# Optimization experiments

Hardware: AMD Instinct MI355X
Metric: run time of the kernel (lower is better)

Reference implementation:

```python
import jax, jax.numpy as jnp
import numpy as np

E, K = 8, 2            # num_experts, top_k
D, H = 1024, 4096      # d_model, expert_hidden_dim
B, S = 4, 2048         # batch, seq
AUX_W = 0.01


def setup_inputs() -> dict:
    key = jax.random.key(0)
    k0, k1, k2, k3 = jax.random.split(key, 4)
    return {
        "x": jax.random.normal(k0, (B, S, D), jnp.float32),
        "router_w": jax.random.normal(k1, (D, E), jnp.float32) * 0.02,  # normal(0.02) init per MoERouter
        "router_b": jnp.zeros((E,), jnp.float32),
        "w_up": jax.random.normal(k2, (E, D, H), jnp.float32) * (1.0 / np.sqrt(D)),
        "b_up": jnp.zeros((E, H), jnp.float32),
        "w_down": jax.random.normal(k3, (E, H, D), jnp.float32) * (1.0 / np.sqrt(H)),
        "b_down": jnp.zeros((E, D), jnp.float32),
    }


def reference(x, router_w, router_b, w_up, b_up, w_down, b_down):
    # Router
    logits = x @ router_w + router_b                       # (B,S,E)
    router_probs = jax.nn.softmax(logits, axis=-1)         # (B,S,E)
    topk_logits, topk_idx = jax.lax.top_k(logits, K)       # (B,S,K)
    topk_p = jax.nn.softmax(topk_logits, axis=-1)          # (B,S,K)

    # Dense all-expert MLP (matches original: every expert computed on every token)
    h = jax.nn.gelu(jnp.einsum('bsd,edh->bseh', x, w_up) + b_up)   # (B,S,E,H)
    all_out = jnp.einsum('bseh,ehd->bsed', h, w_down) + b_down     # (B,S,E,D)

    # Top-k gather + weighted combine
    sel = jnp.take_along_axis(all_out, topk_idx[..., None], axis=2)  # (B,S,K,D)
    output = jnp.sum(topk_p[..., None] * sel, axis=2)                # (B,S,D)

    # Load-balancing aux loss (Switch/Mixtral formulation)
    counts = jnp.zeros((E,), jnp.float32).at[topk_idx.reshape(-1)].add(1.0)
    fraction = counts / (B * S * K)
    prob_mean = router_probs.mean(axis=(0, 1))
    aux_loss = E * jnp.sum(fraction * prob_mean) * AUX_W
    return output, aux_loss, router_probs
```

## Files before the change

kernel.cpp:

```cpp
#include <hip/hip_runtime.h>
#include <hip/hip_bf16.h>
#include <stdint.h>

constexpr int NT = 8192;
constexpr int NE = 8;
constexpr int ND = 1024;
constexpr int NH = 4096;

constexpr int TM = 128;
constexpr int TN = 256;
constexpr int BK = 32;

typedef __attribute__((ext_vector_type(8))) short short8;
typedef __attribute__((ext_vector_type(4))) float f32x4;

constexpr size_t O_XBF  = 0;
constexpr size_t O_WUPT = O_XBF  + (size_t)NT * ND * 2;
constexpr size_t O_WDNT = O_WUPT + (size_t)NE * NH * ND * 2;
constexpr size_t O_HBUF = O_WDNT + (size_t)NE * ND * NH * 2;
constexpr size_t O_STOK = O_HBUF + (size_t)NT * 2 * NH * 2;
constexpr size_t O_SP   = O_STOK + (size_t)NT * 2 * 4;
constexpr size_t O_TKE  = O_SP   + (size_t)NT * 2 * 4;
constexpr size_t O_TKP  = O_TKE  + (size_t)NT * 2 * 4;
constexpr size_t O_CTRL = O_TKP  + (size_t)NT * 2 * 4;
constexpr size_t O_TLUP = O_CTRL + 272;
constexpr size_t O_TLDN = O_TLUP + 160 * 4;

__device__ __forceinline__ void gl_lds16(const void* g, void* l) {
  using GP = char __attribute__((address_space(1))) *;
  using LP = char __attribute__((address_space(3))) *;
  __builtin_amdgcn_global_load_lds((GP)(uintptr_t)g, (LP)(uint32_t)(uintptr_t)l, 16, 0, 0);
}

__device__ __forceinline__ float fast_gelu(float x) {
  float u  = 0.7978845608028654f * (x + 0.044715f * x * x * x);
  float ex = __expf(2.0f * u);
  float th = 1.0f - 2.0f / (ex + 1.0f);
  return 0.5f * x * (1.0f + th);
}

__global__ __launch_bounds__(256) void moe_router(
    const float* __restrict__ x, const float* __restrict__ rw, const float* __restrict__ rb,
    __hip_bfloat16* __restrict__ xbf,
    float* __restrict__ probs_out, int* __restrict__ topk_e, float* __restrict__ topk_p,
    int* __restrict__ cnt_ek, float* __restrict__ probsum)
{
  __shared__ float ps[NE];
  __shared__ int cs[16];
  const int tid = threadIdx.x;
  if (tid < NE) ps[tid] = 0.f;
  if (tid < 16) cs[tid] = 0;
  __syncthreads();
  const int lane = tid & 63, wv = tid >> 6;
  for (int it = 0; it < 8; ++it) {
    const int t = blockIdx.x * 4 + wv + it * 1024;
    const float* xr = x + (size_t)t * ND;
    float acc[NE] = {};
#pragma unroll 4
    for (int j = 0; j < 16; ++j) {
      const int d = j * 64 + lane;
      const float xv = xr[d];
      xbf[(size_t)t * ND + d] = __float2bfloat16(xv);
      const float* w = rw + (size_t)d * NE;
#pragma unroll
      for (int ee = 0; ee < NE; ++ee) acc[ee] += xv * w[ee];
    }
#pragma unroll
    for (int ee = 0; ee < NE; ++ee)
#pragma unroll
      for (int off = 32; off >= 1; off >>= 1)
        acc[ee] += __shfl_down(acc[ee], off, 64);
    if (lane == 0) {
      float lg[NE];
#pragma unroll
      for (int ee = 0; ee < NE; ++ee) lg[ee] = acc[ee] + rb[ee];
      float mx = lg[0];
#pragma unroll
      for (int ee = 1; ee < NE; ++ee) mx = fmaxf(mx, lg[ee]);
      float s = 0.f, pe[NE];
#pragma unroll
      for (int ee = 0; ee < NE; ++ee) { pe[ee] = __expf(lg[ee] - mx); s += pe[ee]; }
      const float inv = 1.f / s;
#pragma unroll
      for (int ee = 0; ee < NE; ++ee) {
        const float pr = pe[ee] * inv;
        probs_out[(size_t)t * NE + ee] = pr;
        atomicAdd(&ps[ee], pr);
      }
      int i1 = 0; float l1 = lg[0];
#pragma unroll
      for (int ee = 1; ee < NE; ++ee) if (lg[ee] > l1) { l1 = lg[ee]; i1 = ee; }
      int i2 = 0; float l2 = -3.0e38f;
#pragma unroll
      for (int ee = 0; ee < NE; ++ee) if (ee != i1 && lg[ee] > l2) { l2 = lg[ee]; i2 = ee; }
      const float e2 = __expf(l2 - l1);
      const float dn = 1.f + e2;
      topk_e[t * 2]     = i1;  topk_e[t * 2 + 1] = i2;
      topk_p[t * 2]     = 1.f / dn;
      topk_p[t * 2 + 1] = e2 / dn;
      atomicAdd(&cs[i1 * 2], 1);
      atomicAdd(&cs[i2 * 2 + 1], 1);
    }
  }
  __syncthreads();
  if (tid < NE) atomicAdd(&probsum[tid], ps[tid]);
  if (tid < 16) atomicAdd(&cnt_ek[tid], cs[tid]);
}

__global__ void moe_finalize(const int* __restrict__ cnt_ek, int* __restrict__ off_ek,
                             const float* __restrict__ probsum, float* __restrict__ aux_out,
                             int* __restrict__ ntiles, int* __restrict__ tl_up,
                             int* __restrict__ tl_dn)
{
  __shared__ int c[16], off[16], uoff[8], ucnt[8], doff[16], dcnt[16];
  const int tid = threadIdx.x;
  if (tid < 16) c[tid] = cnt_ek[tid];
  __syncthreads();
  if (tid == 0) {
    int run = 0;
    for (int i = 0; i < 16; ++i) { off[i] = run; run += c[i]; }
    int ur = 0;
    for (int e = 0; e < NE; ++e) {
      ucnt[e] = (c[2 * e] + c[2 * e + 1] + TM - 1) / TM;
      uoff[e] = ur; ur += ucnt[e];
    }
    ntiles[0] = ur;
    int dr = 0;
    for (int i = 0; i < 16; ++i) {
      dcnt[i] = (c[i] + TM - 1) / TM;
      doff[i] = dr; dr += dcnt[i];
    }
    ntiles[1] = dr;
    float aux = 0.f;
    for (int e = 0; e < NE; ++e) {
      float frac = (float)(c[2 * e] + c[2 * e + 1]) / (float)(NT * 2);
      aux += frac * (probsum[e] / (float)NT);
    }
    aux_out[0] = (float)NE * aux * 0.01f;
  }
  __syncthreads();
  if (tid < 16) off_ek[tid] = off[tid];
  if (tid < 8)
    for (int mb = 0; mb < ucnt[tid]; ++mb) tl_up[uoff[tid] + mb] = (tid << 16) | mb;
  if (tid >= 32 && tid < 48) {
    const int i = tid - 32;
    for (int mb = 0; mb < dcnt[i]; ++mb) tl_dn[doff[i] + mb] = (i << 16) | mb;
  }
}

__global__ __launch_bounds__(256) void moe_scatter(
    const int* __restrict__ topk_e, const float* __restrict__ topk_p,
    const int* __restrict__ off_ek, int* __restrict__ fill_ek,
    int* __restrict__ slot_token, float* __restrict__ slot_p)
{
  __shared__ int lc[16], gb[16], offs[16];
  const int tid = threadIdx.x;
  if (tid < 16) lc[tid] = 0;
  __syncthreads();
  const int t = blockIdx.x * 256 + tid;
  const int id0 = topk_e[t * 2] * 2;
  const int id1 = topk_e[t * 2 + 1] * 2 + 1;
  atomicAdd(&lc[id0], 1);
  atomicAdd(&lc[id1], 1);
  __syncthreads();
  if (tid < 16) {
    gb[tid] = atomicAdd(&fill_ek[tid], lc[tid]);
    offs[tid] = off_ek[tid];
    lc[tid] = 0;
  }
  __syncthreads();
  {
    const int r = atomicAdd(&lc[id0], 1);
    const int slot = offs[id0] + gb[id0] + r;
    slot_token[slot] = t;
    slot_p[slot] = topk_p[t * 2];
  }
  {
    const int r = atomicAdd(&lc[id1], 1);
    const int slot = offs[id1] + gb[id1] + r;
    slot_token[slot] = t;
    slot_p[slot] = topk_p[t * 2 + 1];
  }
}

__global__ __launch_bounds__(256) void moe_transpose_cast(
    const float* __restrict__ in, __hip_bfloat16* __restrict__ outp, int Adim, int Bdim)
{
  __shared__ unsigned short tile[64 * 66];
  const int e = blockIdx.z;
  const int b0 = blockIdx.x * 64, a0 = blockIdx.y * 64;
  const float* ip = in + (size_t)e * Adim * Bdim + (size_t)a0 * Bdim + b0;
  const int c4 = (threadIdx.x & 15) * 4;
  const int r0 = threadIdx.x >> 4;
#pragma unroll
  for (int i = 0; i < 4; ++i) {
    const int r = r0 + i * 16;
    const float4 v = *(const float4*)(ip + (size_t)r * Bdim + c4);
    ushort4 u;
    u.x = __hip_bfloat16_raw(__float2bfloat16(v.x)).x;
    u.y = __hip_bfloat16_raw(__float2bfloat16(v.y)).x;
    u.z = __hip_bfloat16_raw(__float2bfloat16(v.z)).x;
    u.w = __hip_bfloat16_raw(__float2bfloat16(v.w)).x;
    *(ushort4*)&tile[r * 66 + c4] = u;
  }
  __syncthreads();
  unsigned short* op = (unsigned short*)outp + (size_t)e * Bdim * Adim + (size_t)b0 * Adim + a0;
  const int cc  = threadIdx.x >> 2;
  const int rr0 = (threadIdx.x & 3) * 16;
  unsigned short u[16];
#pragma unroll
  for (int i = 0; i < 16; ++i) u[i] = tile[(rr0 + i) * 66 + cc];
  *(short8*)(op + (size_t)cc * Adim + rr0)     = *(short8*)&u[0];
  *(short8*)(op + (size_t)cc * Adim + rr0 + 8) = *(short8*)&u[8];
}

__global__ __launch_bounds__(512, 4) void moe_gemm_up(
    const __hip_bfloat16* __restrict__ xbf,
    const __hip_bfloat16* __restrict__ wupT,
    const float* __restrict__ b_up,
    const int* __restrict__ slot_token,
    const int* __restrict__ cnt_ek, const int* __restrict__ off_ek,
    const int* __restrict__ ntiles, const int* __restrict__ tl_up,
    __hip_bfloat16* __restrict__ hbuf)
{
  if ((int)blockIdx.y >= ntiles[0]) return;
  const int tl = tl_up[blockIdx.y];
  const int e = tl >> 16, mb = tl & 0xffff;
  const int cnt = cnt_ek[2 * e] + cnt_ek[2 * e + 1];
  const int base = off_ek[2 * e];
  const int m0 = mb * TM;
  const int n0 = blockIdx.x * TN;
  const int valid = (cnt - m0 < TM) ? (cnt - m0) : TM;

  __shared__ __align__(16) __hip_bfloat16 As[TM * BK];
  __shared__ __align__(16) __hip_bfloat16 Bs[TN * BK];

  const int tid = threadIdx.x;
  const int lane = tid & 63, wv = tid >> 6;

  const int raA = tid >> 2;
  const int kcA = ((tid & 3) ^ ((raA >> 1) & 3)) * 8;
  int srA = m0 + raA; if (srA >= cnt) srA = cnt - 1;
  const __hip_bfloat16* ga = xbf + (size_t)slot_token[base + srA] * ND + kcA;
  const __hip_bfloat16* gb[2];
#pragma unroll
  for (int j = 0; j < 2; ++j) {
    const int ci = tid + 512 * j;
    const int row = ci >> 2;
    const int kc = ((ci & 3) ^ ((row >> 1) & 3)) * 8;
    gb[j] = wupT + ((size_t)e * NH + n0 + row) * ND + kc;
  }
  char* lA = (char*)As + tid * 16;
  char* lB = (char*)Bs + tid * 16;

  const int wm = (wv >> 2) * 64, wn = (wv & 3) * 64;
  const int l15 = lane & 15, q = lane >> 4;
  const int ssw = (q ^ ((l15 >> 1) & 3)) * 16;
  const char* rA = (const char*)As + (wm + l15) * 64 + ssw;
  const char* rB = (const char*)Bs + (wn + l15) * 64 + ssw;

  f32x4 acc[4][4] = {};

  for (int kk = 0; kk < ND; kk += BK) {
    __syncthreads();
    gl_lds16(ga + kk, lA);
    gl_lds16(gb[0] + kk, lB);
    gl_lds16(gb[1] + kk, lB + 8192);
    __syncthreads();
    short8 af[4], bfr[4];
#pragma unroll
    for (int i = 0; i < 4; ++i) af[i]  = *(const short8*)(rA + i * 1024);
#pragma unroll
    for (int i = 0; i < 4; ++i) bfr[i] = *(const short8*)(rB + i * 1024);
#pragma unroll
    for (int mt = 0; mt < 4; ++mt)
#pragma unroll
      for (int nt = 0; nt < 4; ++nt)
        acc[mt][nt] = __builtin_amdgcn_mfma_f32_16x16x32_bf16(af[mt], bfr[nt], acc[mt][nt], 0, 0, 0);
  }

  float bias[4];
#pragma unroll
  for (int nt = 0; nt < 4; ++nt) bias[nt] = b_up[e * NH + n0 + wn + nt * 16 + l15];
#pragma unroll
  for (int mt = 0; mt < 4; ++mt) {
#pragma unroll
    for (int rr = 0; rr < 4; ++rr) {
      const int row = wm + mt * 16 + q * 4 + rr;
      if (row < valid) {
        const size_t rbase = (size_t)(base + m0 + row) * NH;
#pragma unroll
        for (int nt = 0; nt < 4; ++nt) {
          const int col = n0 + wn + nt * 16 + l15;
          hbuf[rbase + col] = __float2bfloat16(fast_gelu(acc[mt][nt][rr] + bias[nt]));
        }
      }
    }
  }
}

__global__ __launch_bounds__(512, 4) void moe_gemm_down(
    const __hip_bfloat16* __restrict__ hbuf,
    const __hip_bfloat16* __restrict__ wdnT,
    const float* __restrict__ b_down,
    const int* __restrict__ slot_token, const float* __restrict__ slot_p,
    const int* __restrict__ cnt_ek, const int* __restrict__ off_ek,
    const int* __restrict__ ntiles, const int* __restrict__ tl_dn,
    float* __restrict__ out)
{
  if ((int)blockIdx.y >= ntiles[1]) return;
  const int tl = tl_dn[blockIdx.y];
  const int id = tl >> 16, mb = tl & 0xffff;
  const int e = id >> 1;
  const int cnt = cnt_ek[id];
  const int base = off_ek[id];
  const int m0 = mb * TM;
  const int n0 = blockIdx.x * TN;
  const int valid = (cnt - m0 < TM) ? (cnt - m0) : TM;

  __shared__ __align__(16) __hip_bfloat16 As[TM * BK];
  __shared__ __align__(16) __hip_bfloat16 Bs[TN * BK];

  const int tid = threadIdx.x;
  const int lane = tid & 63, wv = tid >> 6;

  const int raA = tid >> 2;
  const int kcA = ((tid & 3) ^ ((raA >> 1) & 3)) * 8;
  int srA = m0 + raA; if (srA >= cnt) srA = cnt - 1;
  const __hip_bfloat16* ga = hbuf + (size_t)(base + srA) * NH + kcA;
  const __hip_bfloat16* gb[2];
#pragma unroll
  for (int j = 0; j < 2; ++j) {
    const int ci = tid + 512 * j;
    const int row = ci >> 2;
    const int kc = ((ci & 3) ^ ((row >> 1) & 3)) * 8;
    gb[j] = wdnT + ((size_t)e * ND + n0 + row) * NH + kc;
  }
  char* lA = (char*)As + tid * 16;
  char* lB = (char*)Bs + tid * 16;

  const int wm = (wv >> 2) * 64, wn = (wv & 3) * 64;
  const int l15 = lane & 15, q = lane >> 4;
  const int ssw = (q ^ ((l15 >> 1) & 3)) * 16;
  const char* rA = (const char*)As + (wm + l15) * 64 + ssw;
  const char* rB = (const char*)Bs + (wn + l15) * 64 + ssw;

  f32x4 acc[4][4] = {};

  for (int kk = 0; kk < NH; kk += BK) {
    __syncthreads();
    gl_lds16(ga + kk, lA);
    gl_lds16(gb[0] + kk, lB);
    gl_lds16(gb[1] + kk, lB + 8192);
    __syncthreads();
    short8 af[4], bfr[4];
#pragma unroll
    for (int i = 0; i < 4; ++i) af[i]  = *(const short8*)(rA + i * 1024);
#pragma unroll
    for (int i = 0; i < 4; ++i) bfr[i] = *(const short8*)(rB + i * 1024);
#pragma unroll
    for (int mt = 0; mt < 4; ++mt)
#pragma unroll
      for (int nt = 0; nt < 4; ++nt)
        acc[mt][nt] = __builtin_amdgcn_mfma_f32_16x16x32_bf16(af[mt], bfr[nt], acc[mt][nt], 0, 0, 0);
  }

  float bias[4];
#pragma unroll
  for (int nt = 0; nt < 4; ++nt) bias[nt] = b_down[e * ND + n0 + wn + nt * 16 + l15];
#pragma unroll
  for (int mt = 0; mt < 4; ++mt) {
#pragma unroll
    for (int rr = 0; rr < 4; ++rr) {
      const int row = wm + mt * 16 + q * 4 + rr;
      if (row < valid) {
        const int slot = base + m0 + row;
        const int tok = slot_token[slot];
        const float p = slot_p[slot];
        const size_t obase = (size_t)tok * ND;
#pragma unroll
        for (int nt = 0; nt < 4; ++nt) {
          const int col = n0 + wn + nt * 16 + l15;
          atomicAdd(&out[obase + col], (acc[mt][nt][rr] + bias[nt]) * p);
        }
      }
    }
  }
}

extern "C" void kernel_launch(void* const* d_in, const int* in_sizes, int n_in,
                              void* d_out, int out_size, void* d_ws, size_t ws_size,
                              hipStream_t stream) {
  (void)in_sizes; (void)n_in; (void)out_size; (void)ws_size;
  const float* x   = (const float*)d_in[0];
  const float* rw  = (const float*)d_in[1];
  const float* rb  = (const float*)d_in[2];
  const float* wup = (const float*)d_in[3];
  const float* bup = (const float*)d_in[4];
  const float* wdn = (const float*)d_in[5];
  const float* bdn = (const float*)d_in[6];
  float* out = (float*)d_out;

  char* ws = (char*)d_ws;
  __hip_bfloat16* xbf  = (__hip_bfloat16*)(ws + O_XBF);
  __hip_bfloat16* wupT = (__hip_bfloat16*)(ws + O_WUPT);
  __hip_bfloat16* wdnT = (__hip_bfloat16*)(ws + O_WDNT);
  __hip_bfloat16* hbuf = (__hip_bfloat16*)(ws + O_HBUF);
  int*   slot_token = (int*)(ws + O_STOK);
  float* slot_p     = (float*)(ws + O_SP);
  int*   topk_e     = (int*)(ws + O_TKE);
  float* topk_p     = (float*)(ws + O_TKP);
  int*   cnt_ek  = (int*)(ws + O_CTRL);
  int*   fill_ek = (int*)(ws + O_CTRL + 64);
  float* probsum = (float*)(ws + O_CTRL + 128);
  int*   off_ek  = (int*)(ws + O_CTRL + 192);
  int*   ntiles  = (int*)(ws + O_CTRL + 256);
  int*   tl_up   = (int*)(ws + O_TLUP);
  int*   tl_dn   = (int*)(ws + O_TLDN);

  hipMemsetAsync(ws + O_CTRL, 0, 272, stream);
  hipMemsetAsync(out, 0, (size_t)NT * ND * sizeof(float), stream);

  moe_transpose_cast<<<dim3(NH / 64, ND / 64, NE), 256, 0, stream>>>(wup, wupT, ND, NH);
  moe_transpose_cast<<<dim3(ND / 64, NH / 64, NE), 256, 0, stream>>>(wdn, wdnT, NH, ND);

  moe_router<<<256, 256, 0, stream>>>(x, rw, rb, xbf, out + (size_t)NT * ND + 1,
                                      topk_e, topk_p, cnt_ek, probsum);
  moe_finalize<<<1, 64, 0, stream>>>(cnt_ek, off_ek, probsum, out + (size_t)NT * ND,
                                     ntiles, tl_up, tl_dn);
  moe_scatter<<<NT / 256, 256, 0, stream>>>(topk_e, topk_p, off_ek, fill_ek, slot_token, slot_p);

  moe_gemm_up<<<dim3(NH / TN, 136, 1), 512, 0, stream>>>(
      xbf, wupT, bup, slot_token, cnt_ek, off_ek, ntiles, tl_up, hbuf);
  moe_gemm_down<<<dim3(ND / TN, 144, 1), 512, 0, stream>>>(
      hbuf, wdnT, bdn, slot_token, slot_p, cnt_ek, off_ek, ntiles, tl_dn, out);
}
```

Baseline: 916.1 us.

## Double-buffer LDS in both expert GEMMs and split-K the down projection

Both grouped GEMM kernels now use two LDS buffers, so the next K-slice is issued while MFMAs run on the current one, and each iteration needs one barrier instead of two. The down-projection GEMM also splits its K dimension (4096) across two blocks via blockIdx.z, with only the first split adding the bias, and both splits accumulate into the output with atomics. The aim is to hide global load latency and, for the down GEMM (only 4 column tiles wide), to put more blocks on the GPU. The cost is double the LDS per block, which may lower occupancy, and twice as many atomic adds on the output.

New measurement: 884.1 us. -3.5%, faster.

```diff
diff --git a/kernel.cpp b/kernel.cpp
--- a/kernel.cpp
+++ b/kernel.cpp
@@ -10,6 +10,7 @@
 constexpr int TM = 128;
 constexpr int TN = 256;
 constexpr int BK = 32;
+constexpr int KS_DN = 2;
 
 typedef __attribute__((ext_vector_type(8))) short short8;
 typedef __attribute__((ext_vector_type(4))) float f32x4;
@@ -232,8 +233,8 @@
   const int n0 = blockIdx.x * TN;
   const int valid = (cnt - m0 < TM) ? (cnt - m0) : TM;
 
-  __shared__ __align__(16) __hip_bfloat16 As[TM * BK];
-  __shared__ __align__(16) __hip_bfloat16 Bs[TN * BK];
+  __shared__ __align__(16) __hip_bfloat16 As0[TM * BK], As1[TM * BK];
+  __shared__ __align__(16) __hip_bfloat16 Bs0[TN * BK], Bs1[TN * BK];
 
   const int tid = threadIdx.x;
   const int lane = tid & 63, wv = tid >> 6;
@@ -242,41 +243,60 @@
   const int kcA = ((tid & 3) ^ ((raA >> 1) & 3)) * 8;
   int srA = m0 + raA; if (srA >= cnt) srA = cnt - 1;
   const __hip_bfloat16* ga = xbf + (size_t)slot_token[base + srA] * ND + kcA;
-  const __hip_bfloat16* gb[2];
-#pragma unroll
-  for (int j = 0; j < 2; ++j) {
-    const int ci = tid + 512 * j;
-    const int row = ci >> 2;
-    const int kc = ((ci & 3) ^ ((row >> 1) & 3)) * 8;
-    gb[j] = wupT + ((size_t)e * NH + n0 + row) * ND + kc;
-  }
-  char* lA = (char*)As + tid * 16;
-  char* lB = (char*)Bs + tid * 16;
+  const __hip_bfloat16* gb0;
+  const __hip_bfloat16* gb1;
+  {
+    const int r0 = tid >> 2;
+    const int k0 = ((tid & 3) ^ ((r0 >> 1) & 3)) * 8;
+    gb0 = wupT + ((size_t)e * NH + n0 + r0) * ND + k0;
+    const int ci = tid + 512;
+    const int r1 = ci >> 2;
+    const int k1 = ((ci & 3) ^ ((r1 >> 1) & 3)) * 8;
+    gb1 = wupT + ((size_t)e * NH + n0 + r1) * ND + k1;
+  }
+  char* lA0 = (char*)As0 + tid * 16;
+  char* lA1 = (char*)As1 + tid * 16;
+  char* lB0 = (char*)Bs0 + tid * 16;
+  char* lB1 = (char*)Bs1 + tid * 16;
 
   const int wm = (wv >> 2) * 64, wn = (wv & 3) * 64;
   const int l15 = lane & 15, q = lane >> 4;
   const int ssw = (q ^ ((l15 >> 1) & 3)) * 16;
-  const char* rA = (const char*)As + (wm + l15) * 64 + ssw;
-  const char* rB = (const char*)Bs + (wn + l15) * 64 + ssw;
+  const char* rA0 = (const char*)As0 + (wm + l15) * 64 + ssw;
+  const char* rA1 = (const char*)As1 + (wm + l15) * 64 + ssw;
+  const char* rB0 = (const char*)Bs0 + (wn + l15) * 64 + ssw;
+  const char* rB1 = (const char*)Bs1 + (wn + l15) * 64 + ssw;
 
   f32x4 acc[4][4] = {};
 
-  for (int kk = 0; kk < ND; kk += BK) {
-    __syncthreads();
-    gl_lds16(ga + kk, lA);
-    gl_lds16(gb[0] + kk, lB);
-    gl_lds16(gb[1] + kk, lB + 8192);
-    __syncthreads();
+  auto STAGE = [&](char* sA, char* sB, int kk) {
+    gl_lds16(ga + kk, sA);
+    gl_lds16(gb0 + kk, sB);
+    gl_lds16(gb1 + kk, sB + 8192);
+  };
+  auto COMPUTE = [&](const char* bA, const char* bB) {
     short8 af[4], bfr[4];
 #pragma unroll
-    for (int i = 0; i < 4; ++i) af[i]  = *(const short8*)(rA + i * 1024);
-#pragma unroll
-    for (int i = 0; i < 4; ++i) bfr[i] = *(const short8*)(rB + i * 1024);
+    for (int i = 0; i < 4; ++i) af[i]  = *(const short8*)(bA + i * 1024);
+#pragma unroll
+    for (int i = 0; i < 4; ++i) bfr[i] = *(const short8*)(bB + i * 1024);
 #pragma unroll
     for (int mt = 0; mt < 4; ++mt)
 #pragma unroll
       for (int nt = 0; nt < 4; ++nt)
         acc[mt][nt] = __builtin_amdgcn_mfma_f32_16x16x32_bf16(af[mt], bfr[nt], acc[mt][nt], 0, 0, 0);
+  };
+
+  STAGE(lA0, lB0, 0);
+  __syncthreads();
+
+  for (int kk = 0; kk < ND; kk += 2 * BK) {
+    STAGE(lA1, lB1, kk + BK);
+    COMPUTE(rA0, rB0);
+    __syncthreads();
+    if (kk + 2 * BK < ND) STAGE(lA0, lB0, kk + 2 * BK);
+    COMPUTE(rA1, rB1);
+    __syncthreads();
   }
 
   float bias[4];
@@ -317,9 +337,12 @@
   const int m0 = mb * TM;
   const int n0 = blockIdx.x * TN;
   const int valid = (cnt - m0 < TM) ? (cnt - m0) : TM;
-
-  __shared__ __align__(16) __hip_bfloat16 As[TM * BK];
-  __shared__ __align__(16) __hip_bfloat16 Bs[TN * BK];
+  const int ks = blockIdx.z;
+  const int k_beg = ks * (NH / KS_DN);
+  const int k_end = k_beg + (NH / KS_DN);
+
+  __shared__ __align__(16) __hip_bfloat16 As0[TM * BK], As1[TM * BK];
+  __shared__ __align__(16) __hip_bfloat16 Bs0[TN * BK], Bs1[TN * BK];
 
   const int tid = threadIdx.x;
   const int lane = tid & 63, wv = tid >> 6;
@@ -328,46 +351,66 @@
   const int kcA = ((tid & 3) ^ ((raA >> 1) & 3)) * 8;
   int srA = m0 + raA; if (srA >= cnt) srA = cnt - 1;
   const __hip_bfloat16* ga = hbuf + (size_t)(base + srA) * NH + kcA;
-  const __hip_bfloat16* gb[2];
-#pragma unroll
-  for (int j = 0; j < 2; ++j) {
-    const int ci = tid + 512 * j;
-    const int row = ci >> 2;
-    const int kc = ((ci & 3) ^ ((row >> 1) & 3)) * 8;
-    gb[j] = wdnT + ((size_t)e * ND + n0 + row) * NH + kc;
-  }
-  char* lA = (char*)As + tid * 16;
-  char* lB = (char*)Bs + tid * 16;
+  const __hip_bfloat16* gb0;
+  const __hip_bfloat16* gb1;
+  {
+    const int r0 = tid >> 2;
+    const int k0 = ((tid & 3) ^ ((r0 >> 1) & 3)) * 8;
+    gb0 = wdnT + ((size_t)e * ND + n0 + r0) * NH + k0;
+    const int ci = tid + 512;
+    const int r1 = ci >> 2;
+    const int k1 = ((ci & 3) ^ ((r1 >> 1) & 3)) * 8;
+    gb1 = wdnT + ((size_t)e * ND + n0 + r1) * NH + k1;
+  }
+  char* lA0 = (char*)As0 + tid * 16;
+  char* lA1 = (char*)As1 + tid * 16;
+  char* lB0 = (char*)Bs0 + tid * 16;
+  char* lB1 = (char*)Bs1 + tid * 16;
 
   const int wm = (wv >> 2) * 64, wn = (wv & 3) * 64;
   const int l15 = lane & 15, q = lane >> 4;
   const int ssw = (q ^ ((l15 >> 1) & 3)) * 16;
-  const char* rA = (const char*)As + (wm + l15) * 64 + ssw;
-  const char* rB = (const char*)Bs + (wn + l15) * 64 + ssw;
+  const char* rA0 = (const char*)As0 + (wm + l15) * 64 + ssw;
+  const char* rA1 = (const char*)As1 + (wm + l15) * 64 + ssw;
+  const char* rB0 = (const char*)Bs0 + (wn + l15) * 64 + ssw;
+  const char* rB1 = (const char*)Bs1 + (wn + l15) * 64 + ssw;
 
   f32x4 acc[4][4] = {};
 
-  for (int kk = 0; kk < NH; kk += BK) {
-    __syncthreads();
-    gl_lds16(ga + kk, lA);
-    gl_lds16(gb[0] + kk, lB);
-    gl_lds16(gb[1] + kk, lB + 8192);
-    __syncthreads();
+  auto STAGE = [&](char* sA, char* sB, int kk) {
+    gl_lds16(ga + kk, sA);
+    gl_lds16(gb0 + kk, sB);
+    gl_lds16(gb1 + kk, sB + 8192);
+  };
+  auto COMPUTE = [&](const char* bA, const char* bB) {
     short8 af[4], bfr[4];
 #pragma unroll
-    for (int i = 0; i < 4; ++i) af[i]  = *(const short8*)(rA + i * 1024);
-#pragma unroll
-    for (int i = 0; i < 4; ++i) bfr[i] = *(const short8*)(rB + i * 1024);
+    for (int i = 0; i < 4; ++i) af[i]  = *(const short8*)(bA + i * 1024);
+#pragma unroll
+    for (int i = 0; i < 4; ++i) bfr[i] = *(const short8*)(bB + i * 1024);
 #pragma unroll
     for (int mt = 0; mt < 4; ++mt)
 #pragma unroll
       for (int nt = 0; nt < 4; ++nt)
         acc[mt][nt] = __builtin_amdgcn_mfma_f32_16x16x32_bf16(af[mt], bfr[nt], acc[mt][nt], 0, 0, 0);
+  };
+
+  STAGE(lA0, lB0, k_beg);
+  __syncthreads();
+
+  for (int kk = k_beg; kk < k_end; kk += 2 * BK) {
+    STAGE(lA1, lB1, kk + BK);
+    COMPUTE(rA0, rB0);
+    __syncthreads();
+    if (kk + 2 * BK < k_end) STAGE(lA0, lB0, kk + 2 * BK);
+    COMPUTE(rA1, rB1);
+    __syncthreads();
   }
 
   float bias[4];
 #pragma unroll
-  for (int nt = 0; nt < 4; ++nt) bias[nt] = b_down[e * ND + n0 + wn + nt * 16 + l15];
+  for (int nt = 0; nt < 4; ++nt)
+    bias[nt] = (ks == 0) ? b_down[e * ND + n0 + wn + nt * 16 + l15] : 0.f;
 #pragma unroll
   for (int mt = 0; mt < 4; ++mt) {
 #pragma unroll
@@ -432,6 +475,6 @@
 
   moe_gemm_up<<<dim3(NH / TN, 136, 1), 512, 0, stream>>>(
       xbf, wupT, bup, slot_token, cnt_ek, off_ek, ntiles, tl_up, hbuf);
-  moe_gemm_down<<<dim3(ND / TN, 144, 1), 512, 0, stream>>>(
+  moe_gemm_down<<<dim3(ND / TN, 144, KS_DN), 512, 0, stream>>>(
       hbuf, wdnT, bdn, slot_token, slot_p, cnt_ek, off_ek, ntiles, tl_dn, out);
 }
```

## Enlarge GEMM tiles, add 4-stage LDS pipeline, split-K the down projection

Applied to the files above, without the earlier changes.

Both expert GEMMs now use 256x256 tiles with each wave computing 128x64. The k-loop becomes a 4-buffer LDS ring that loads two stages ahead, with explicit vmcnt waits, a single barrier per step and raised priority around the MFMA block. The down GEMM gains a 2-way split-K over the grid z dimension, relying on the existing atomic output adds and adding the bias only in the first split. The aim is to hide global-load latency, raise arithmetic intensity and keep enough blocks in flight, at the cost of more LDS (128KB per block), higher register pressure, lower occupancy and doubled atomic traffic in the down GEMM.

After: 868.7 us. 1.05x faster.

```diff
diff --git a/kernel.cpp b/kernel.cpp
--- a/kernel.cpp
+++ b/kernel.cpp
@@ -7,9 +7,11 @@
 constexpr int ND = 1024;
 constexpr int NH = 4096;
 
-constexpr int TM = 128;
-constexpr int TN = 256;
+constexpr int BM = 256;
+constexpr int BN = 256;
 constexpr int BK = 32;
+constexpr int NBUF = 4;
+constexpr int KS_DN = 2;
 
 typedef __attribute__((ext_vector_type(8))) short short8;
 typedef __attribute__((ext_vector_type(4))) float f32x4;
@@ -121,13 +123,13 @@
     for (int i = 0; i < 16; ++i) { off[i] = run; run += c[i]; }
     int ur = 0;
     for (int e = 0; e < NE; ++e) {
-      ucnt[e] = (c[2 * e] + c[2 * e + 1] + TM - 1) / TM;
+      ucnt[e] = (c[2 * e] + c[2 * e + 1] + BM - 1) / BM;
       uoff[e] = ur; ur += ucnt[e];
     }
     ntiles[0] = ur;
     int dr = 0;
     for (int i = 0; i < 16; ++i) {
-      dcnt[i] = (c[i] + TM - 1) / TM;
+      dcnt[i] = (c[i] + BM - 1) / BM;
       doff[i] = dr; dr += dcnt[i];
     }
     ntiles[1] = dr;
@@ -214,7 +216,8 @@
   *(short8*)(op + (size_t)cc * Adim + rr0 + 8) = *(short8*)&u[8];
 }
 
-__global__ __launch_bounds__(512, 4) void moe_gemm_up(
+
+__global__ __launch_bounds__(512, 2) void moe_gemm_up(
     const __hip_bfloat16* __restrict__ xbf,
     const __hip_bfloat16* __restrict__ wupT,
     const float* __restrict__ b_up,
@@ -228,62 +231,81 @@
   const int e = tl >> 16, mb = tl & 0xffff;
   const int cnt = cnt_ek[2 * e] + cnt_ek[2 * e + 1];
   const int base = off_ek[2 * e];
-  const int m0 = mb * TM;
-  const int n0 = blockIdx.x * TN;
-  const int valid = (cnt - m0 < TM) ? (cnt - m0) : TM;
-
-  __shared__ __align__(16) __hip_bfloat16 As[TM * BK];
-  __shared__ __align__(16) __hip_bfloat16 Bs[TN * BK];
+  const int m0 = mb * BM;
+  const int n0 = blockIdx.x * BN;
+  const int valid = (cnt - m0 < BM) ? (cnt - m0) : BM;
+
+  __shared__ __align__(16) __hip_bfloat16 As[NBUF][BM * BK];
+  __shared__ __align__(16) __hip_bfloat16 Bs[NBUF][BN * BK];
 
   const int tid = threadIdx.x;
   const int lane = tid & 63, wv = tid >> 6;
 
-  const int raA = tid >> 2;
-  const int kcA = ((tid & 3) ^ ((raA >> 1) & 3)) * 8;
-  int srA = m0 + raA; if (srA >= cnt) srA = cnt - 1;
-  const __hip_bfloat16* ga = xbf + (size_t)slot_token[base + srA] * ND + kcA;
-  const __hip_bfloat16* gb[2];
-#pragma unroll
-  for (int j = 0; j < 2; ++j) {
-    const int ci = tid + 512 * j;
-    const int row = ci >> 2;
-    const int kc = ((ci & 3) ^ ((row >> 1) & 3)) * 8;
-    gb[j] = wupT + ((size_t)e * NH + n0 + row) * ND + kc;
-  }
-  char* lA = (char*)As + tid * 16;
-  char* lB = (char*)Bs + tid * 16;
-
-  const int wm = (wv >> 2) * 64, wn = (wv & 3) * 64;
+  const int r0c = tid >> 2;
+  const int k0c = ((tid & 3) ^ ((r0c >> 1) & 3)) * 8;
+  const int r1c = r0c + 128;
+  const int k1c = ((tid & 3) ^ ((r1c >> 1) & 3)) * 8;
+  int srA0 = m0 + r0c; if (srA0 >= cnt) srA0 = cnt - 1;
+  int srA1 = m0 + r1c; if (srA1 >= cnt) srA1 = cnt - 1;
+  const __hip_bfloat16* gA0 = xbf + (size_t)slot_token[base + srA0] * ND + k0c;
+  const __hip_bfloat16* gA1 = xbf + (size_t)slot_token[base + srA1] * ND + k1c;
+  const __hip_bfloat16* gB0 = wupT + ((size_t)e * NH + n0 + r0c) * ND + k0c;
+  const __hip_bfloat16* gB1 = wupT + ((size_t)e * NH + n0 + r1c) * ND + k1c;
+
+  auto STAGE = [&](int bi, int kk) {
+    char* sA = (char*)&As[bi][0] + tid * 16;
+    char* sB = (char*)&Bs[bi][0] + tid * 16;
+    gl_lds16(gA0 + kk, sA);
+    gl_lds16(gA1 + kk, sA + 8192);
+    gl_lds16(gB0 + kk, sB);
+    gl_lds16(gB1 + kk, sB + 8192);
+  };
+
+  const int wm = (wv >> 2) * 128, wn = (wv & 3) * 64;
   const int l15 = lane & 15, q = lane >> 4;
   const int ssw = (q ^ ((l15 >> 1) & 3)) * 16;
-  const char* rA = (const char*)As + (wm + l15) * 64 + ssw;
-  const char* rB = (const char*)Bs + (wn + l15) * 64 + ssw;
-
-  f32x4 acc[4][4] = {};
-
-  for (int kk = 0; kk < ND; kk += BK) {
-    __syncthreads();
-    gl_lds16(ga + kk, lA);
-    gl_lds16(gb[0] + kk, lB);
-    gl_lds16(gb[1] + kk, lB + 8192);
-    __syncthreads();
-    short8 af[4], bfr[4];
-#pragma unroll
-    for (int i = 0; i < 4; ++i) af[i]  = *(const short8*)(rA + i * 1024);
-#pragma unroll
-    for (int i = 0; i < 4; ++i) bfr[i] = *(const short8*)(rB + i * 1024);
-#pragma unroll
-    for (int mt = 0; mt < 4; ++mt)
+
+  f32x4 acc[8][4] = {};
+
+  auto COMPUTE = [&](int bi) {
+    const char* bA = (const char*)&As[bi][0] + (wm + l15) * 64 + ssw;
+    const char* bB = (const char*)&Bs[bi][0] + (wn + l15) * 64 + ssw;
+    short8 af[8], bfr[4];
+#pragma unroll
+    for (int i = 0; i < 8; ++i) af[i]  = *(const short8*)(bA + i * 1024);
+#pragma unroll
+    for (int i = 0; i < 4; ++i) bfr[i] = *(const short8*)(bB + i * 1024);
+    __builtin_amdgcn_s_setprio(1);
+#pragma unroll
+    for (int mt = 0; mt < 8; ++mt)
 #pragma unroll
       for (int nt = 0; nt < 4; ++nt)
         acc[mt][nt] = __builtin_amdgcn_mfma_f32_16x16x32_bf16(af[mt], bfr[nt], acc[mt][nt], 0, 0, 0);
+    __builtin_amdgcn_s_setprio(0);
+  };
+
+  constexpr int KT = ND / BK;
+  STAGE(0, 0);
+  STAGE(1, BK);
+  for (int t = 0; t < KT; ++t) {
+    if (t + 2 < KT) {
+      STAGE((t + 2) & 3, (t + 2) * BK);
+      asm volatile("s_waitcnt vmcnt(8)" ::: "memory");
+    } else if (t + 2 == KT) {
+      asm volatile("s_waitcnt vmcnt(4)" ::: "memory");
+    } else {
+      asm volatile("s_waitcnt vmcnt(0)" ::: "memory");
+    }
+    __builtin_amdgcn_s_barrier();
+    __builtin_amdgcn_sched_barrier(0);
+    COMPUTE(t & 3);
   }
 
   float bias[4];
 #pragma unroll
   for (int nt = 0; nt < 4; ++nt) bias[nt] = b_up[e * NH + n0 + wn + nt * 16 + l15];
 #pragma unroll
-  for (int mt = 0; mt < 4; ++mt) {
+  for (int mt = 0; mt < 8; ++mt) {
 #pragma unroll
     for (int rr = 0; rr < 4; ++rr) {
       const int row = wm + mt * 16 + q * 4 + rr;
@@ -299,7 +321,7 @@
   }
 }
 
-__global__ __launch_bounds__(512, 4) void moe_gemm_down(
+__global__ __launch_bounds__(512, 2) void moe_gemm_down(
     const __hip_bfloat16* __restrict__ hbuf,
     const __hip_bfloat16* __restrict__ wdnT,
     const float* __restrict__ b_down,
@@ -314,62 +336,84 @@
   const int e = id >> 1;
   const int cnt = cnt_ek[id];
   const int base = off_ek[id];
-  const int m0 = mb * TM;
-  const int n0 = blockIdx.x * TN;
-  const int valid = (cnt - m0 < TM) ? (cnt - m0) : TM;
-
-  __shared__ __align__(16) __hip_bfloat16 As[TM * BK];
-  __shared__ __align__(16) __hip_bfloat16 Bs[TN * BK];
+  const int m0 = mb * BM;
+  const int n0 = blockIdx.x * BN;
+  const int valid = (cnt - m0 < BM) ? (cnt - m0) : BM;
+  const int ks = blockIdx.z;
+  const int k_beg = ks * (NH / KS_DN);
+
+  __shared__ __align__(16) __hip_bfloat16 As[NBUF][BM * BK];
+  __shared__ __align__(16) __hip_bfloat16 Bs[NBUF][BN * BK];
 
   const int tid = threadIdx.x;
   const int lane = tid & 63, wv = tid >> 6;
 
-  const int raA = tid >> 2;
-  const int kcA = ((tid & 3) ^ ((raA >> 1) & 3)) * 8;
-  int srA = m0 + raA; if (srA >= cnt) srA = cnt - 1;
-  const __hip_bfloat16* ga = hbuf + (size_t)(base + srA) * NH + kcA;
-  const __hip_bfloat16* gb[2];
-#pragma unroll
-  for (int j = 0; j < 2; ++j) {
-    const int ci = tid + 512 * j;
-    const int row = ci >> 2;
-    const int kc = ((ci & 3) ^ ((row >> 1) & 3)) * 8;
-    gb[j] = wdnT + ((size_t)e * ND + n0 + row) * NH + kc;
-  }
-  char* lA = (char*)As + tid * 16;
-  char* lB = (char*)Bs + tid * 16;
-
-  const int wm = (wv >> 2) * 64, wn = (wv & 3) * 64;
+  const int r0c = tid >> 2;
+  const int k0c = ((tid & 3) ^ ((r0c >> 1) & 3)) * 8;
+  const int r1c = r0c + 128;
+  const int k1c = ((tid & 3) ^ ((r1c >> 1) & 3)) * 8;
+  int srA0 = m0 + r0c; if (srA0 >= cnt) srA0 = cnt - 1;
+  int srA1 = m0 + r1c; if (srA1 >= cnt) srA1 = cnt - 1;
+  const __hip_bfloat16* gA0 = hbuf + (size_t)(base + srA0) * NH + k0c;
+  const __hip_bfloat16* gA1 = hbuf + (size_t)(base + srA1) * NH + k1c;
+  const __hip_bfloat16* gB0 = wdnT + ((size_t)e * ND + n0 + r0c) * NH + k0c;
+  const __hip_bfloat16* gB1 = wdnT + ((size_t)e * ND + n0 + r1c) * NH + k1c;
+
+  auto STAGE = [&](int bi, int kk) {
+    char* sA = (char*)&As[bi][0] + tid * 16;
+    char* sB = (char*)&Bs[bi][0] + tid * 16;
+    gl_lds16(gA0 + kk, sA);
+    gl_lds16(gA1 + kk, sA + 8192);
+    gl_lds16(gB0 + kk, sB);
+    gl_lds16(gB1 + kk, sB + 8192);
+  };
+
+  const int wm = (wv >> 2) * 128, wn = (wv & 3) * 64;
   const int l15 = lane & 15, q = lane >> 4;
   const int ssw = (q ^ ((l15 >> 1) & 3)) * 16;
-  const char* rA = (const char*)As + (wm + l15) * 64 + ssw;
-  const char* rB = (const char*)Bs + (wn + l15) * 64 + ssw;
-
-  f32x4 acc[4][4] = {};
-
-  for (int kk = 0; kk < NH; kk += BK) {
-    __syncthreads();
-    gl_lds16(ga + kk, lA);
-    gl_lds16(gb[0] + kk, lB);
-    gl_lds16(gb[1] + kk, lB + 8192);
-    __syncthreads();
-    short8 af[4], bfr[4];
-#pragma unroll
-    for (int i = 0; i < 4; ++i) af[i]  = *(const short8*)(rA + i * 1024);
-#pragma unroll
-    for (int i = 0; i < 4; ++i) bfr[i] = *(const short8*)(rB + i * 1024);
-#pragma unroll
-    for (int mt = 0; mt < 4; ++mt)
+
+  f32x4 acc[8][4] = {};
+
+  auto COMPUTE = [&](int bi) {
+    const char* bA = (const char*)&As[bi][0] + (wm + l15) * 64 + ssw;
+    const char* bB = (const char*)&Bs[bi][0] + (wn + l15) * 64 + ssw;
+    short8 af[8], bfr[4];
+#pragma unroll
+    for (int i = 0; i < 8; ++i) af[i]  = *(const short8*)(bA + i * 1024);
+#pragma unroll
+    for (int i = 0; i < 4; ++i) bfr[i] = *(const short8*)(bB + i * 1024);
+    __builtin_amdgcn_s_setprio(1);
+#pragma unroll
+    for (int mt = 0; mt < 8; ++mt)
 #pragma unroll
       for (int nt = 0; nt < 4; ++nt)
         acc[mt][nt] = __builtin_amdgcn_mfma_f32_16x16x32_bf16(af[mt], bfr[nt], acc[mt][nt], 0, 0, 0);
+    __builtin_amdgcn_s_setprio(0);
+  };
+
+  constexpr int KT = (NH / KS_DN) / BK;
+  STAGE(0, k_beg);
+  STAGE(1, k_beg + BK);
+  for (int t = 0; t < KT; ++t) {
+    if (t + 2 < KT) {
+      STAGE((t + 2) & 3, k_beg + (t + 2) * BK);
+      asm volatile("s_waitcnt vmcnt(8)" ::: "memory");
+    } else if (t + 2 == KT) {
+      asm volatile("s_waitcnt vmcnt(4)" ::: "memory");
+    } else {
+      asm volatile("s_waitcnt vmcnt(0)" ::: "memory");
+    }
+    __builtin_amdgcn_s_barrier();
+    __builtin_amdgcn_sched_barrier(0);
+    COMPUTE(t & 3);
   }
 
   float bias[4];
 #pragma unroll
-  for (int nt = 0; nt < 4; ++nt) bias[nt] = b_down[e * ND + n0 + wn + nt * 16 + l15];
-#pragma unroll
-  for (int mt = 0; mt < 4; ++mt) {
+  for (int nt = 0; nt < 4; ++nt)
+    bias[nt] = (ks == 0) ? b_down[e * ND + n0 + wn + nt * 16 + l15] : 0.f;
+#pragma unroll
+  for (int mt = 0; mt < 8; ++mt) {
 #pragma unroll
     for (int rr = 0; rr < 4; ++rr) {
       const int row = wm + mt * 16 + q * 4 + rr;
@@ -430,8 +474,8 @@
                                      ntiles, tl_up, tl_dn);
   moe_scatter<<<NT / 256, 256, 0, stream>>>(topk_e, topk_p, off_ek, fill_ek, slot_token, slot_p);
 
-  moe_gemm_up<<<dim3(NH / TN, 136, 1), 512, 0, stream>>>(
+  moe_gemm_up<<<dim3(NH / BN, 72, 1), 512, 0, stream>>>(
       xbf, wupT, bup, slot_token, cnt_ek, off_ek, ntiles, tl_up, hbuf);
-  moe_gemm_down<<<dim3(ND / TN, 144, 1), 512, 0, stream>>>(
+  moe_gemm_down<<<dim3(ND / BN, 80, KS_DN), 512, 0, stream>>>(
       hbuf, wdnT, bdn, slot_token, slot_p, cnt_ek, off_ek, ntiles, tl_dn, out);
 }
```
